# Kernel tuning notes

Hardware: AMD Instinct MI355X
Metric: run time of the kernel (lower is better)

Reference implementation:

```python
import jax, jax.numpy as jnp
import numpy as np

B, T, D = 4, 8192, 512
H, BS = 8, 16


def setup_inputs() -> dict:
    key = jax.random.key(0)
    ks = jax.random.split(key, 7)
    s = 1.0 / np.sqrt(D)
    return {
        "x": jax.random.normal(ks[0], (B, T, D), dtype=jnp.float32),
        "Wq": jax.random.normal(ks[1], (D, D), dtype=jnp.float32) * s,
        "bq": jax.random.normal(ks[2], (D,), dtype=jnp.float32) * 0.02,
        "Wk": jax.random.normal(ks[3], (D, D), dtype=jnp.float32) * s,
        "bk": jax.random.normal(ks[4], (D,), dtype=jnp.float32) * 0.02,
        "Wv": jax.random.normal(ks[5], (D, D), dtype=jnp.float32) * s,
        "bv": jax.random.normal(ks[6], (D,), dtype=jnp.float32) * 0.02,
    }


def reference(x, Wq, bq, Wk, bk, Wv, bv):
    b, t, d_model = x.shape
    nb = t // BS          # number of blocks
    dh = d_model // H     # per-head dim
    # [B,T,D] -> [B,nb,BS,D] -> [B,BS,nb,D]: attention runs across blocks
    xb = x.reshape(b, nb, BS, d_model).transpose(0, 2, 1, 3)
    # projections (torch Linear: x @ W.T + b)
    q = xb @ Wq.T + bq
    k = xb @ Wk.T + bk
    v = xb @ Wv.T + bv
    # split heads: [B,BS,nb,H,dh] -> [B,BS,H,nb,dh]
    q = q.reshape(b, BS, nb, H, dh).transpose(0, 1, 3, 2, 4)
    k = k.reshape(b, BS, nb, H, dh).transpose(0, 1, 3, 2, 4)
    v = v.reshape(b, BS, nb, H, dh).transpose(0, 1, 3, 2, 4)
    scale = d_model ** (-0.5)  # note: full dim, as in the original
    attn = jnp.einsum('bshnd,bshmd->bshnm', q, k) * scale  # [B,BS,H,nb,nb]
    attn = jax.nn.softmax(attn, axis=-1)
    out = jnp.einsum('bshnm,bshmd->bshnd', attn, v)        # [B,BS,H,nb,dh]
    # merge heads and undo block permute
    out = out.transpose(0, 1, 3, 2, 4).reshape(b, BS, nb, d_model)
    out = out.transpose(0, 2, 1, 3).reshape(b, t, d_model)
    return out
```

## Files before the change

kernel.cpp:

```cpp
#include <hip/hip_runtime.h>
#include <hip/hip_bf16.h>
#include <cstdint>
#include <cstddef>

#define Bsz 4
#define Tsz 8192
#define Dsz 512
#define Hn 8
#define BSn 16
#define NBn 512
#define DHn 64
#define NQKV 1536
#define MROWS 32768

#define SCL 0.06375870136f
#define ATT_M 8.0f

typedef __attribute__((ext_vector_type(8))) short short8;
typedef __attribute__((ext_vector_type(4))) float float4f;

__device__ __forceinline__ uint16_t f2b(float f) {
  union { float f; uint32_t u; } v; v.f = f;
  uint32_t u = v.u;
  return (uint16_t)((u + 0x7fffu + ((u >> 16) & 1u)) >> 16);
}

__device__ __forceinline__ uint32_t pk2(float a, float b) {
  union { float f; uint32_t u; } x, y; x.f = a; y.f = b;
  return __builtin_amdgcn_perm(y.u + 0x8000u, x.u + 0x8000u, 0x07060302u);
}

__device__ __forceinline__ uint32_t pk2t(float a, float b) {
  union { float f; uint32_t u; } x, y; x.f = a; y.f = b;
  return __builtin_amdgcn_perm(y.u, x.u, 0x07060302u);
}

__device__ __forceinline__ void gl_lds16(const void* g, void* l) {
  __builtin_amdgcn_global_load_lds(
      (const __attribute__((address_space(1))) unsigned int*)g,
      (__attribute__((address_space(3))) unsigned int*)l, 16, 0, 0);
}

#define XBLK (MROWS * Dsz / 1024)
__global__ void cvt_kernel(const float* __restrict__ x, const float* __restrict__ Wq,
                           const float* __restrict__ Wk, const float* __restrict__ Wv,
                           uint16_t* __restrict__ xb, uint16_t* __restrict__ wc) {
  int bid = blockIdx.x;
  if (bid < XBLK) {
    int i = (bid * 256 + threadIdx.x) * 4;
    float4 v = *(const float4*)(x + i);
    uint64_t o = (uint64_t)pk2(v.x, v.y) | ((uint64_t)pk2(v.z, v.w) << 32);
    *(uint64_t*)(xb + i) = o;
  } else {
    int i = ((bid - XBLK) * 256 + threadIdx.x) * 4;
    int row = i >> 9;
    int col = i & 511;
    const float* src = (row < 512) ? Wq : ((row < 1024) ? Wk : Wv);
    float4 v = *(const float4*)(src + (size_t)(row & 511) * 512 + col);
    uint64_t o = (uint64_t)pk2(v.x, v.y) | ((uint64_t)pk2(v.z, v.w) << 32);
    *(uint64_t*)(wc + i) = o;
  }
}

#define BM 128
#define BN 128
#define BK 64

__global__ __launch_bounds__(256) void gemm_qkv(
    const uint16_t* __restrict__ Xb, const uint16_t* __restrict__ Wc,
    const float* __restrict__ bq, const float* __restrict__ bkp,
    const float* __restrict__ bv, uint16_t* __restrict__ Qp,
    uint16_t* __restrict__ Kp, uint16_t* __restrict__ Vtmp) {
  __shared__ uint16_t As[BM * BK];
  __shared__ uint16_t Bs[BN * BK];
  const int tid = threadIdx.x;
  const int wave = tid >> 6, lane = tid & 63;
  const int lrow = lane & 15, quad = lane >> 4;

  int g = blockIdx.x;
  int xcd = g & 7, ii = g >> 3;
  int mt = xcd * 32 + ii / 12;
  int nt = ii - (ii / 12) * 12;
  const int m0 = mt * BM;
  const int n0 = nt * BN;
  const int wm = (wave >> 1) * 64, wn = (wave & 1) * 64;

  float4f acc[4][4] = {};

  for (int k0 = 0; k0 < Dsz; k0 += BK) {
    __syncthreads();
#pragma unroll
    for (int p = 0; p < 4; ++p) {
      int cbase = p * 256 + wave * 64;
      int c = cbase + lane;
      int row = c >> 3, pos = c & 7;
      int kc = (pos ^ (row & 7)) * 8;
      gl_lds16(Xb + (size_t)(m0 + row) * Dsz + k0 + kc, As + cbase * 8);
      gl_lds16(Wc + (size_t)(n0 + row) * Dsz + k0 + kc, Bs + cbase * 8);
    }
    __syncthreads();

#pragma unroll
    for (int h = 0; h < 2; ++h) {
      short8 af[4], bf[4];
#pragma unroll
      for (int i = 0; i < 4; ++i) {
        int rowA = wm + i * 16 + lrow;
        af[i] = *(const short8*)(As + rowA * BK + (((h * 4 + quad) ^ (rowA & 7)) * 8));
        int rowB = wn + i * 16 + lrow;
        bf[i] = *(const short8*)(Bs + rowB * BK + (((h * 4 + quad) ^ (rowB & 7)) * 8));
      }
#pragma unroll
      for (int j = 0; j < 4; ++j)
#pragma unroll
        for (int i = 0; i < 4; ++i)
          acc[j][i] = __builtin_amdgcn_mfma_f32_16x16x32_bf16(bf[j], af[i], acc[j][i], 0, 0, 0);
    }
  }

  const int region = n0 >> 9;
  const float* bias = (region == 0) ? bq : ((region == 1) ? bkp : bv);
  const float mult = (region == 0) ? SCL : 1.0f;
  const int bb = m0 >> 13;
  const int nbbase = ((m0 & 8191) >> 4) + (wm >> 4);
  const int nv0 = (n0 & 511) + wn;

  if (region < 2) {
    uint16_t* dst = (region == 0) ? Qp : Kp;
    const int hh = nv0 >> 6;
    uint16_t* plane = dst + ((((size_t)bb * 16 + lrow) * 8 + hh) << 15);
#pragma unroll
    for (int j = 0; j < 4; ++j) {
      int dh0 = j * 16 + quad * 4;
      float4 bv4 = *(const float4*)(bias + nv0 + dh0);
#pragma unroll
      for (int i = 0; i < 4; ++i) {
        float4f a = acc[j][i];
        uint2 st = make_uint2(pk2((a[0] + bv4.x) * mult, (a[1] + bv4.y) * mult),
                              pk2((a[2] + bv4.z) * mult, (a[3] + bv4.w) * mult));
        *(uint2*)(plane + (size_t)(nbbase + i) * 64 + dh0) = st;
      }
    }
  } else {
#pragma unroll
    for (int j = 0; j < 4; ++j) {
      int c0 = nv0 + j * 16 + quad * 4;
      float4 bv4 = *(const float4*)(bias + c0);
#pragma unroll
      for (int i = 0; i < 4; ++i) {
        int token = m0 + wm + i * 16 + lrow;
        float4f a = acc[j][i];
        uint2 st = make_uint2(pk2(a[0] + bv4.x, a[1] + bv4.y),
                              pk2(a[2] + bv4.z, a[3] + bv4.w));
        *(uint2*)(Vtmp + (size_t)token * 512 + c0) = st;
      }
    }
  }
}

__global__ __launch_bounds__(256) void vtrans(const uint16_t* __restrict__ Vtmp,
                                              uint16_t* __restrict__ Vt) {
  __shared__ uint16_t tile[64 * 64];
  int bx = blockIdx.x;
  const int nt = bx & 7; bx >>= 3;
  const int h = bx & 7; bx >>= 3;
  const int s = bx & 15;
  const int b = bx >> 4;
  const int tid = threadIdx.x;

  {
    int i = tid >> 2;
    int token = b * Tsz + (nt * 64 + i) * BSn + s;
    const uint16_t* src = Vtmp + (size_t)token * 512 + h * 64;
#pragma unroll
    for (int hh = 0; hh < 2; ++hh) {
      int ch = (tid & 3) * 2 + hh;
      short8 v = *(const short8*)(src + ch * 8);
      int pc = ch ^ (i & 7);
      *(short8*)(tile + i * 64 + pc * 8) = v;
    }
  }
  __syncthreads();
  {
    int dh = tid & 63, seg = tid >> 6;
    short8 v1, v2;
#pragma unroll
    for (int k = 0; k < 8; ++k) {
      int nb_l = seg * 16 + k;
      v1[k] = (short)tile[nb_l * 64 + (((dh >> 3) ^ (nb_l & 7)) * 8) + (dh & 7)];
    }
#pragma unroll
    for (int k = 0; k < 8; ++k) {
      int nb_l = seg * 16 + 8 + k;
      v2[k] = (short)tile[nb_l * 64 + (((dh >> 3) ^ (nb_l & 7)) * 8) + (dh & 7)];
    }
    size_t obase = ((((size_t)b * 16 + s) * 8 + h) * 64 + dh) * 512 + nt * 64 + seg * 16;
    *(short8*)(Vt + obase) = v1;
    *(short8*)(Vt + obase + 8) = v2;
  }
}

__global__ __launch_bounds__(256, 3) void attn_kernel(
    const uint16_t* __restrict__ Qp, const uint16_t* __restrict__ Kp,
    const uint16_t* __restrict__ Vt, float* __restrict__ out) {
  __shared__ uint16_t Ks[32 * 64];
  __shared__ uint16_t Vs[64 * 32];
  __shared__ uint16_t Ps[4][4][16 * 32];

  int bx = blockIdx.x;
  const int qh = bx & 1; bx >>= 1;
  const int h = bx & 7; bx >>= 3;
  const int s = bx & 15;
  const int b = bx >> 4;

  const int tid = threadIdx.x;
  const int w = tid >> 6, lane = tid & 63;
  const int lrow = lane & 15, quad = lane >> 4;

  const size_t sh = (((size_t)b * 16 + s) * 8 + h);
  const uint16_t* Qb = Qp + (sh << 15);
  const uint16_t* Kb = Kp + (sh << 15);
  const uint16_t* Vb = Vt + (sh << 15);

  short8 qB[4][2];
  const int q0 = qh * 256 + w * 64;
#pragma unroll
  for (int qs = 0; qs < 4; ++qs) {
    const uint16_t* qp = Qb + (size_t)(q0 + qs * 16 + lrow) * 64;
    qB[qs][0] = *(const short8*)(qp + quad * 8);
    qB[qs][1] = *(const short8*)(qp + 32 + quad * 8);
  }

  float4f O[4][4] = {};
  float l_acc[4] = {0.f, 0.f, 0.f, 0.f};

  const int kr = w * 8 + (lane >> 3);
  const int kcs = (lane & 7) ^ (kr & 7);
  const int vr = w * 16 + (lane >> 2);
  const int vcs = (lane & 3) ^ ((vr >> 1) & 3);

  const int sw = (lrow >> 1) & 3;
  const float4f negm = {-ATT_M, -ATT_M, -ATT_M, -ATT_M};

  for (int kv0 = 0; kv0 < NBn; kv0 += 32) {
    __syncthreads();
    gl_lds16(Kb + (size_t)(kv0 + kr) * 64 + kcs * 8, Ks + w * 512);
    gl_lds16(Vb + (size_t)vr * 512 + kv0 + vcs * 8, Vs + w * 512);
    __syncthreads();

    {
      short8 kA[2][2];
#pragma unroll
      for (int kt = 0; kt < 2; ++kt) {
        int row = kt * 16 + lrow;
#pragma unroll
        for (int kc = 0; kc < 2; ++kc) {
          int cc = (kc * 4 + quad) ^ (row & 7);
          kA[kt][kc] = *(const short8*)(Ks + row * 64 + cc * 8);
        }
      }
#pragma unroll
      for (int qs = 0; qs < 4; ++qs) {
        float4f c0 = negm, c1 = negm;
        c0 = __builtin_amdgcn_mfma_f32_16x16x32_bf16(kA[0][0], qB[qs][0], c0, 0, 0, 0);
        c0 = __builtin_amdgcn_mfma_f32_16x16x32_bf16(kA[0][1], qB[qs][1], c0, 0, 0, 0);
        c1 = __builtin_amdgcn_mfma_f32_16x16x32_bf16(kA[1][0], qB[qs][0], c1, 0, 0, 0);
        c1 = __builtin_amdgcn_mfma_f32_16x16x32_bf16(kA[1][1], qB[qs][1], c1, 0, 0, 0);

        float p00 = __builtin_amdgcn_exp2f(c0[0]);
        float p01 = __builtin_amdgcn_exp2f(c0[1]);
        float p02 = __builtin_amdgcn_exp2f(c0[2]);
        float p03 = __builtin_amdgcn_exp2f(c0[3]);
        float p10 = __builtin_amdgcn_exp2f(c1[0]);
        float p11 = __builtin_amdgcn_exp2f(c1[1]);
        float p12 = __builtin_amdgcn_exp2f(c1[2]);
        float p13 = __builtin_amdgcn_exp2f(c1[3]);
        l_acc[qs] += ((p00 + p01) + (p02 + p03)) + ((p10 + p11) + (p12 + p13));

        uint32_t d0 = pk2t(p00, p01), d1 = pk2t(p02, p03);
        uint32_t d2 = pk2t(p10, p11), d3 = pk2t(p12, p13);
        uint16_t* Psq = Ps[w][qs];
        int half = (quad & 1) * 4;
        *(uint2*)(Psq + lrow * 32 + (((quad >> 1)) ^ sw) * 8 + half) = make_uint2(d0, d1);
        *(uint2*)(Psq + lrow * 32 + ((2 + (quad >> 1)) ^ sw) * 8 + half) = make_uint2(d2, d3);
      }
    }

    {
      short8 vA[4];
#pragma unroll
      for (int dt = 0; dt < 4; ++dt) {
        int row = dt * 16 + lrow;
        vA[dt] = *(const short8*)(Vs + row * 32 + (quad ^ ((row >> 1) & 3)) * 8);
      }
#pragma unroll
      for (int qs = 0; qs < 4; ++qs) {
        short8 pB = *(const short8*)(Ps[w][qs] + lrow * 32 + (quad ^ sw) * 8);
#pragma unroll
        for (int dt = 0; dt < 4; ++dt)
          O[dt][qs] = __builtin_amdgcn_mfma_f32_16x16x32_bf16(vA[dt], pB, O[dt][qs], 0, 0, 0);
      }
    }
  }

#pragma unroll
  for (int qs = 0; qs < 4; ++qs) {
    float l = l_acc[qs];
    l += __shfl_xor(l, 16);
    l += __shfl_xor(l, 32);
    float inv = 1.0f / l;
    int qg = q0 + qs * 16 + lrow;
    float* op = out + ((size_t)b * Tsz + (size_t)qg * 16 + s) * Dsz + h * 64;
#pragma unroll
    for (int dt = 0; dt < 4; ++dt) {
      float4 vv;
      vv.x = O[dt][qs][0] * inv; vv.y = O[dt][qs][1] * inv;
      vv.z = O[dt][qs][2] * inv; vv.w = O[dt][qs][3] * inv;
      *(float4*)(op + dt * 16 + quad * 4) = vv;
    }
  }
}

extern "C" void kernel_launch(void* const* d_in, const int* in_sizes, int n_in,
                              void* d_out, int out_size, void* d_ws, size_t ws_size,
                              hipStream_t stream) {
  const float* x  = (const float*)d_in[0];
  const float* Wq = (const float*)d_in[1];
  const float* bq = (const float*)d_in[2];
  const float* Wk = (const float*)d_in[3];
  const float* bk = (const float*)d_in[4];
  const float* Wv = (const float*)d_in[5];
  const float* bv = (const float*)d_in[6];
  float* out = (float*)d_out;

  uint16_t* Qp   = (uint16_t*)d_ws;
  uint16_t* Kp   = Qp + (size_t)16777216;
  uint16_t* Vtmp = Kp + (size_t)16777216;
  uint16_t* xb   = Vtmp + (size_t)16777216;
  uint16_t* wc   = xb + (size_t)16777216;
  uint16_t* Vt   = xb;

  hipLaunchKernelGGL(cvt_kernel, dim3(XBLK + NQKV * Dsz / 1024), dim3(256), 0, stream,
                     x, Wq, Wk, Wv, xb, wc);
  hipLaunchKernelGGL(gemm_qkv, dim3((MROWS / BM) * (NQKV / BN)), dim3(256), 0, stream,
                     xb, wc, bq, bk, bv, Qp, Kp, Vtmp);
  hipLaunchKernelGGL(vtrans, dim3(Bsz * BSn * Hn * 8), dim3(256), 0, stream, Vtmp, Vt);
  hipLaunchKernelGGL(attn_kernel, dim3(Bsz * BSn * Hn * 2), dim3(256), 0, stream,
                     Qp, Kp, Vt, out);
}
```

Baseline: 277.1 us.

## Halve QKV GEMM N-tile to 64 and swap MFMA operand order

Shrinks the QKV projection GEMM tile from 128x128 to 128x64, doubling the grid to 24 N-tiles per M-tile, and adds an occupancy hint of 6 blocks per CU. The MFMA operand order is swapped so each lane now holds four consecutive token rows for a single output column. The epilogue therefore writes scattered 2-byte bf16 stores instead of packed 8-byte vectors. The aim is more waves in flight and fewer accumulator registers, at the cost of less reuse per tile and much less coalesced output stores.

```diff
diff --git a/kernel.cpp b/kernel.cpp
--- a/kernel.cpp
+++ b/kernel.cpp
@@ -63,10 +63,10 @@
 }
 
 #define BM 128
-#define BN 128
+#define BN 64
 #define BK 64
 
-__global__ __launch_bounds__(256) void gemm_qkv(
+__global__ __launch_bounds__(256, 6) void gemm_qkv(
     const uint16_t* __restrict__ Xb, const uint16_t* __restrict__ Wc,
     const float* __restrict__ bq, const float* __restrict__ bkp,
     const float* __restrict__ bv, uint16_t* __restrict__ Qp,
@@ -79,13 +79,13 @@
 
   int g = blockIdx.x;
   int xcd = g & 7, ii = g >> 3;
-  int mt = xcd * 32 + ii / 12;
-  int nt = ii - (ii / 12) * 12;
+  int mt = xcd * 32 + ii / 24;
+  int nt = ii - (ii / 24) * 24;
   const int m0 = mt * BM;
   const int n0 = nt * BN;
-  const int wm = (wave >> 1) * 64, wn = (wave & 1) * 64;
-
-  float4f acc[4][4] = {};
+  const int wm = (wave >> 1) * 64, wn = (wave & 1) * 32;
+
+  float4f acc[4][2] = {};
 
   for (int k0 = 0; k0 < Dsz; k0 += BK) {
     __syncthreads();
@@ -96,25 +96,35 @@
       int row = c >> 3, pos = c & 7;
       int kc = (pos ^ (row & 7)) * 8;
       gl_lds16(Xb + (size_t)(m0 + row) * Dsz + k0 + kc, As + cbase * 8);
+    }
+#pragma unroll
+    for (int p = 0; p < 2; ++p) {
+      int cbase = p * 256 + wave * 64;
+      int c = cbase + lane;
+      int row = c >> 3, pos = c & 7;
+      int kc = (pos ^ (row & 7)) * 8;
       gl_lds16(Wc + (size_t)(n0 + row) * Dsz + k0 + kc, Bs + cbase * 8);
     }
     __syncthreads();
 
 #pragma unroll
     for (int h = 0; h < 2; ++h) {
-      short8 af[4], bf[4];
+      short8 af[4], bf[2];
 #pragma unroll
       for (int i = 0; i < 4; ++i) {
         int rowA = wm + i * 16 + lrow;
         af[i] = *(const short8*)(As + rowA * BK + (((h * 4 + quad) ^ (rowA & 7)) * 8));
-        int rowB = wn + i * 16 + lrow;
-        bf[i] = *(const short8*)(Bs + rowB * BK + (((h * 4 + quad) ^ (rowB & 7)) * 8));
-      }
-#pragma unroll
-      for (int j = 0; j < 4; ++j)
-#pragma unroll
-        for (int i = 0; i < 4; ++i)
-          acc[j][i] = __builtin_amdgcn_mfma_f32_16x16x32_bf16(bf[j], af[i], acc[j][i], 0, 0, 0);
+      }
+#pragma unroll
+      for (int j = 0; j < 2; ++j) {
+        int rowB = wn + j * 16 + lrow;
+        bf[j] = *(const short8*)(Bs + rowB * BK + (((h * 4 + quad) ^ (rowB & 7)) * 8));
+      }
+#pragma unroll
+      for (int i = 0; i < 4; ++i)
+#pragma unroll
+        for (int j = 0; j < 2; ++j)
+          acc[i][j] = __builtin_amdgcn_mfma_f32_16x16x32_bf16(af[i], bf[j], acc[i][j], 0, 0, 0);
     }
   }
 
@@ -127,32 +137,31 @@
 
   if (region < 2) {
     uint16_t* dst = (region == 0) ? Qp : Kp;
-    const int hh = nv0 >> 6;
-    uint16_t* plane = dst + ((((size_t)bb * 16 + lrow) * 8 + hh) << 15);
-#pragma unroll
-    for (int j = 0; j < 4; ++j) {
-      int dh0 = j * 16 + quad * 4;
-      float4 bv4 = *(const float4*)(bias + nv0 + dh0);
+#pragma unroll
+    for (int j = 0; j < 2; ++j) {
+      int nl = nv0 + j * 16 + lrow;
+      int hh = nl >> 6, dh = nl & 63;
+      float bval = bias[nl];
+      size_t base = (size_t)bb * 4194304 + (size_t)hh * 32768 +
+                    (size_t)nbbase * 64 + dh + (size_t)(quad * 4) * 262144;
+#pragma unroll
+      for (int i = 0; i < 4; ++i)
+#pragma unroll
+        for (int r = 0; r < 4; ++r)
+          dst[base + (size_t)r * 262144 + (size_t)i * 64] =
+              f2b((acc[i][j][r] + bval) * mult);
+    }
+  } else {
+#pragma unroll
+    for (int j = 0; j < 2; ++j) {
+      int nl = nv0 + j * 16 + lrow;
+      float bval = bias[nl];
 #pragma unroll
       for (int i = 0; i < 4; ++i) {
-        float4f a = acc[j][i];
-        uint2 st = make_uint2(pk2((a[0] + bv4.x) * mult, (a[1] + bv4.y) * mult),
-                              pk2((a[2] + bv4.z) * mult, (a[3] + bv4.w) * mult));
-        *(uint2*)(plane + (size_t)(nbbase + i) * 64 + dh0) = st;
-      }
-    }
-  } else {
-#pragma unroll
-    for (int j = 0; j < 4; ++j) {
-      int c0 = nv0 + j * 16 + quad * 4;
-      float4 bv4 = *(const float4*)(bias + c0);
-#pragma unroll
-      for (int i = 0; i < 4; ++i) {
-        int token = m0 + wm + i * 16 + lrow;
-        float4f a = acc[j][i];
-        uint2 st = make_uint2(pk2(a[0] + bv4.x, a[1] + bv4.y),
-                              pk2(a[2] + bv4.z, a[3] + bv4.w));
-        *(uint2*)(Vtmp + (size_t)token * 512 + c0) = st;
+        int tok = m0 + wm + i * 16 + quad * 4;
+#pragma unroll
+        for (int r = 0; r < 4; ++r)
+          Vtmp[(size_t)(tok + r) * 512 + nl] = f2b(acc[i][j][r] + bval);
       }
     }
   }
```

After: 254.1 us. 8.3% less time.
